# Kernel optimization log

Measured on AMD Instinct MI355X. Metric: run time of the kernel, lower is better.

## Reference

```python
import jax, jax.numpy as jnp
import numpy as np

NUM_ROUTES = 12800   # 32 * 20 * 20
NUM_CAPS = 25
IN_CH = 8
OUT_CH = 64
BATCH = 8
NUM_ITERS = 3


def setup_inputs() -> dict:
    key = jax.random.key(0)
    kx, kw = jax.random.split(key)
    x = jax.random.normal(kx, (BATCH, NUM_ROUTES, IN_CH), dtype=jnp.float32)
    # W parameter: torch shape [1, R, C, O, I] -> store as [R, C, O, I]
    W = jax.random.normal(kw, (NUM_ROUTES, NUM_CAPS, OUT_CH, IN_CH), dtype=jnp.float32)
    return {"x": x, "W": W}


def _squash_elementwise(s):
    # Faithful to source: squared_norm sums over last dim of s_j which has size 1,
    # so squash acts elementwise: s^2 * s / ((1+s^2) * |s|) = s*|s|/(1+s^2).
    sq = s * s
    return sq * s / ((1.0 + sq) * jnp.sqrt(sq))


def reference(x, W):
    # u_hat[b,r,c,o] = sum_i W[r,c,o,i] * x[b,r,i]
    u_hat = jnp.einsum('rcoi,bri->brco', W, x)  # [B, R, C, O]
    b_ij = jnp.zeros((NUM_ROUTES, NUM_CAPS), dtype=x.dtype)
    v = None
    for it in range(NUM_ITERS):
        # legacy F.softmax on 4D [1,R,C,1] uses implicit dim=1 -> over routes
        c_ij = jax.nn.softmax(b_ij, axis=0)                  # [R, C]
        s = jnp.einsum('rc,brco->bco', c_ij, u_hat)          # [B, C, O]
        v = _squash_elementwise(s)
        if it < NUM_ITERS - 1:
            # agreement: <u_hat, v> per (b,r,c), then mean over batch
            a = jnp.einsum('brco,bco->brc', u_hat, v)
            b_ij = b_ij + jnp.mean(a, axis=0)
    # torch returns v_j.squeeze(1) with shape [B, C, O, 1]
    return v[..., None]
```

## Files before the change

kernel.cpp:

```cpp
#include <hip/hip_runtime.h>
#include <cstdint>
#include <cstddef>

#define RN 12800
#define CN 25
#define ON 64
#define IN_ 8
#define BN 8
#define SOUT (BN*CN*ON)

#define RPC 64
#define NRC (RN / RPC)

__device__ __forceinline__ uint32_t pack_bf16(float a, float b) {
    uint32_t ua = __float_as_uint(a);
    uint32_t ub = __float_as_uint(b);
    ua = (ua + 0x7fffu + ((ua >> 16) & 1u)) >> 16;
    ub = (ub + 0x7fffu + ((ub >> 16) & 1u)) & 0xffff0000u;
    return ua | ub;
}
__device__ __forceinline__ float lo_bf16(uint32_t q) { return __uint_as_float(q << 16); }
__device__ __forceinline__ float hi_bf16(uint32_t q) { return __uint_as_float(q & 0xffff0000u); }

__global__ void __launch_bounds__(320, 6)
caps_pass0(const float* __restrict__ x, const float* __restrict__ W,
           float* __restrict__ Sp, uint32_t* __restrict__ U)
{
    __shared__ float xs[RPC][BN][IN_];
    const int chunk = blockIdx.y;
    const int r0 = chunk * RPC;

    for (int t = threadIdx.x; t < RPC * BN * 2; t += 320) {
        const int i4 = t & 1;
        const int rl = (t >> 1) & (RPC - 1);
        const int b  = t >> 7;
        const float4 val = *reinterpret_cast<const float4*>(
            x + (((size_t)b * RN + r0 + rl) * IN_) + i4 * 4);
        *reinterpret_cast<float4*>(&xs[rl][b][i4 * 4]) = val;
    }
    __syncthreads();

    const int wave = threadIdx.x >> 6;
    const int lane = threadIdx.x & 63;
    const int c = blockIdx.x * 5 + wave;

    float acc[BN];
    #pragma unroll
    for (int b = 0; b < BN; ++b) acc[b] = 0.f;

    #pragma unroll 2
    for (int rl = 0; rl < RPC; ++rl) {
        const int r = r0 + rl;
        const float4* wp = reinterpret_cast<const float4*>(
            W + ((((size_t)r * CN + c) * ON + lane) * IN_));
        const float4 w0 = wp[0];
        const float4 w1 = wp[1];

        float u[BN];
        #pragma unroll
        for (int b = 0; b < BN; ++b) {
            const float4 xa = *reinterpret_cast<const float4*>(&xs[rl][b][0]);
            const float4 xb = *reinterpret_cast<const float4*>(&xs[rl][b][4]);
            u[b] = w0.x*xa.x + w0.y*xa.y + w0.z*xa.z + w0.w*xa.w
                 + w1.x*xb.x + w1.y*xb.y + w1.z*xb.z + w1.w*xb.w;
            acc[b] += u[b];
        }

        uint4 q;
        q.x = pack_bf16(u[0], u[1]);
        q.y = pack_bf16(u[2], u[3]);
        q.z = pack_bf16(u[4], u[5]);
        q.w = pack_bf16(u[6], u[7]);
        *reinterpret_cast<uint4*>(U + (((size_t)r * CN + c) * ON + lane) * 4) = q;
    }

    float* sp = Sp + (size_t)chunk * SOUT;
    #pragma unroll
    for (int b = 0; b < BN; ++b)
        sp[(b * CN + c) * ON + lane] = acc[b];
}

template<int MODE>
__global__ void __launch_bounds__(320, 6)
caps_passU(const uint32_t* __restrict__ U, const float* __restrict__ vin,
           const float* __restrict__ bin, float* __restrict__ bout,
           float* __restrict__ Sp, float* __restrict__ Zp)
{
    const int chunk = blockIdx.y;
    const int r0 = chunk * RPC;
    const int wave = threadIdx.x >> 6;
    const int lane = threadIdx.x & 63;
    const int c = blockIdx.x * 5 + wave;

    float vreg[BN];
    #pragma unroll
    for (int b = 0; b < BN; ++b)
        vreg[b] = vin[(b * CN + c) * ON + lane];

    float acc[BN];
    #pragma unroll
    for (int b = 0; b < BN; ++b) acc[b] = 0.f;
    float zacc = 0.f;

    #pragma unroll 2
    for (int rl = 0; rl < RPC; ++rl) {
        const int r = r0 + rl;
        const uint4 q = *reinterpret_cast<const uint4*>(
            U + (((size_t)r * CN + c) * ON + lane) * 4);
        float u[BN];
        u[0] = lo_bf16(q.x); u[1] = hi_bf16(q.x);
        u[2] = lo_bf16(q.y); u[3] = hi_bf16(q.y);
        u[4] = lo_bf16(q.z); u[5] = hi_bf16(q.z);
        u[6] = lo_bf16(q.w); u[7] = hi_bf16(q.w);

        float p = 0.f;
        #pragma unroll
        for (int b = 0; b < BN; ++b) p += u[b] * vreg[b];
        #pragma unroll
        for (int off = 32; off > 0; off >>= 1) p += __shfl_xor(p, off, 64);

        float bn = p * (1.0f / BN);
        if (MODE == 2) bn += bin[(size_t)r * CN + c];
        if (MODE == 1 && lane == 0) bout[(size_t)r * CN + c] = bn;
        const float e = __expf(bn);
        zacc += e;
        #pragma unroll
        for (int b = 0; b < BN; ++b) acc[b] += e * u[b];
    }

    float* sp = Sp + (size_t)chunk * SOUT;
    #pragma unroll
    for (int b = 0; b < BN; ++b)
        sp[(b * CN + c) * ON + lane] = acc[b];
    if (lane == 0)
        Zp[chunk * 32 + c] = zacc;
}

__global__ void caps_zred(const float* __restrict__ Zp, float* __restrict__ z)
{
    __shared__ float l[256];
    const int t = threadIdx.x;
    const int cc = t >> 3;
    const int g  = t & 7;
    float s = 0.f;
    if (cc < CN)
        for (int j = g; j < NRC; j += 8) s += Zp[j * 32 + cc];
    l[t] = s;
    __syncthreads();
    if (g == 0 && cc < CN) {
        float ss = 0.f;
        #pragma unroll
        for (int k = 0; k < 8; ++k) ss += l[cc * 8 + k];
        z[cc] = ss;
    }
}

template<int PASS>
__global__ void __launch_bounds__(256)
caps_fin(const float* __restrict__ Sp, const float* __restrict__ z,
         float* __restrict__ vout)
{
    __shared__ float l[256];
    const int blk = blockIdx.x;
    const int t = threadIdx.x;
    const int o = t & 63;
    const int g = t >> 6;
    const int base = blk * 64 + o;
    float s = 0.f;
    for (int w = g * 50; w < g * 50 + 50; ++w)
        s += Sp[(size_t)w * SOUT + base];
    l[t] = s;
    __syncthreads();
    if (g == 0) {
        float ss = l[o] + l[64 + o] + l[128 + o] + l[192 + o];
        const float zz = (PASS == 0) ? (float)RN : z[blk % CN];
        ss /= zz;
        vout[base] = ss * fabsf(ss) / (1.f + ss * ss);
    }
}

extern "C" void kernel_launch(void* const* d_in, const int* in_sizes, int n_in,
                              void* d_out, int out_size, void* d_ws, size_t ws_size,
                              hipStream_t stream)
{
    const float* x = (const float*)d_in[0];
    const float* W = (const float*)d_in[1];
    float* out = (float*)d_out;
    float* ws = (float*)d_ws;

    float* v  = ws;
    float* z  = v + SOUT;
    float* b1 = z + 32;
    float* Zp = b1 + (size_t)RN * CN;
    float* Sp = Zp + (size_t)NRC * 32;
    uint32_t* U = (uint32_t*)(Sp + (size_t)NRC * SOUT);

    dim3 blk(320), grid(5, NRC);
    dim3 fblk(256), fgrid(BN * CN);

    caps_pass0<<<grid, blk, 0, stream>>>(x, W, Sp, U);
    caps_fin<0><<<fgrid, fblk, 0, stream>>>(Sp, z, v);
    caps_passU<1><<<grid, blk, 0, stream>>>(U, v, nullptr, b1, Sp, Zp);
    caps_zred<<<1, 256, 0, stream>>>(Zp, z);
    caps_fin<1><<<fgrid, fblk, 0, stream>>>(Sp, z, v);
    caps_passU<2><<<grid, blk, 0, stream>>>(U, v, b1, nullptr, Sp, Zp);
    caps_zred<<<1, 256, 0, stream>>>(Zp, z);
    caps_fin<2><<<fgrid, fblk, 0, stream>>>(Sp, z, out);
}
```

Baseline: 384.1 us.

## Fuse all routing passes into one cooperative persistent kernel with grid syncs

Replaces the eight separate kernel launches with a single cooperative persistent kernel that runs the pass0, finalize and routing phases in a grid-stride loop, separated by grid.sync(). The z-normalizer reduction is folded into the finalize phase. W and U accesses now use nontemporal loads and stores. The aim is to remove launch gaps and tail effects between the short phases, at the cost of grid-wide barriers and limited occupancy. A multi-kernel fallback is kept.

```diff
diff --git a/kernel.cpp b/kernel.cpp
--- a/kernel.cpp
+++ b/kernel.cpp
@@ -1,6 +1,9 @@
 #include <hip/hip_runtime.h>
+#include <hip/hip_cooperative_groups.h>
 #include <cstdint>
 #include <cstddef>
+
+namespace cg = cooperative_groups;
 
 #define RN 12800
 #define CN 25
@@ -11,6 +14,11 @@
 
 #define RPC 64
 #define NRC (RN / RPC)
+#define NWU (5 * NRC)
+#define NFIN (BN * CN)
+
+typedef float    f4x  __attribute__((ext_vector_type(4)));
+typedef uint32_t u4x  __attribute__((ext_vector_type(4)));
 
 __device__ __forceinline__ uint32_t pack_bf16(float a, float b) {
     uint32_t ua = __float_as_uint(a);
@@ -22,161 +30,198 @@
 __device__ __forceinline__ float lo_bf16(uint32_t q) { return __uint_as_float(q << 16); }
 __device__ __forceinline__ float hi_bf16(uint32_t q) { return __uint_as_float(q & 0xffff0000u); }
 
-__global__ void __launch_bounds__(320, 6)
-caps_pass0(const float* __restrict__ x, const float* __restrict__ W,
-           float* __restrict__ Sp, uint32_t* __restrict__ U)
-{
-    __shared__ float xs[RPC][BN][IN_];
-    const int chunk = blockIdx.y;
-    const int r0 = chunk * RPC;
-
-    for (int t = threadIdx.x; t < RPC * BN * 2; t += 320) {
-        const int i4 = t & 1;
-        const int rl = (t >> 1) & (RPC - 1);
-        const int b  = t >> 7;
-        const float4 val = *reinterpret_cast<const float4*>(
-            x + (((size_t)b * RN + r0 + rl) * IN_) + i4 * 4);
-        *reinterpret_cast<float4*>(&xs[rl][b][i4 * 4]) = val;
-    }
-    __syncthreads();
-
-    const int wave = threadIdx.x >> 6;
-    const int lane = threadIdx.x & 63;
-    const int c = blockIdx.x * 5 + wave;
-
-    float acc[BN];
-    #pragma unroll
-    for (int b = 0; b < BN; ++b) acc[b] = 0.f;
-
-    #pragma unroll 2
-    for (int rl = 0; rl < RPC; ++rl) {
-        const int r = r0 + rl;
-        const float4* wp = reinterpret_cast<const float4*>(
-            W + ((((size_t)r * CN + c) * ON + lane) * IN_));
-        const float4 w0 = wp[0];
-        const float4 w1 = wp[1];
-
-        float u[BN];
-        #pragma unroll
-        for (int b = 0; b < BN; ++b) {
-            const float4 xa = *reinterpret_cast<const float4*>(&xs[rl][b][0]);
-            const float4 xb = *reinterpret_cast<const float4*>(&xs[rl][b][4]);
-            u[b] = w0.x*xa.x + w0.y*xa.y + w0.z*xa.z + w0.w*xa.w
-                 + w1.x*xb.x + w1.y*xb.y + w1.z*xb.z + w1.w*xb.w;
-            acc[b] += u[b];
-        }
-
-        uint4 q;
-        q.x = pack_bf16(u[0], u[1]);
-        q.y = pack_bf16(u[2], u[3]);
-        q.z = pack_bf16(u[4], u[5]);
-        q.w = pack_bf16(u[6], u[7]);
-        *reinterpret_cast<uint4*>(U + (((size_t)r * CN + c) * ON + lane) * 4) = q;
-    }
-
-    float* sp = Sp + (size_t)chunk * SOUT;
-    #pragma unroll
-    for (int b = 0; b < BN; ++b)
-        sp[(b * CN + c) * ON + lane] = acc[b];
+union SMem {
+    float xs[RPC][BN][IN_];
+    float red[320];
+};
+
+__device__ __forceinline__ void phase_pass0(
+    const float* __restrict__ x, const float* __restrict__ W,
+    float* __restrict__ Sp, uint32_t* __restrict__ U,
+    SMem& sm, int nb, int bid)
+{
+    const int t = threadIdx.x, wave = t >> 6, lane = t & 63;
+    for (int wu = bid; wu < NWU; wu += nb) {
+        const int chunk = wu % NRC, bx = wu / NRC;
+        const int r0 = chunk * RPC;
+        const int c = bx * 5 + wave;
+        __syncthreads();
+        for (int s = t; s < RPC * BN * 2; s += 320) {
+            const int i4 = s & 1, rl = (s >> 1) & (RPC - 1), b = s >> 7;
+            *reinterpret_cast<float4*>(&sm.xs[rl][b][i4 * 4]) =
+                *reinterpret_cast<const float4*>(
+                    x + (((size_t)b * RN + r0 + rl) * IN_) + i4 * 4);
+        }
+        __syncthreads();
+
+        float acc[BN];
+        #pragma unroll
+        for (int b = 0; b < BN; ++b) acc[b] = 0.f;
+
+        #pragma unroll 2
+        for (int rl = 0; rl < RPC; ++rl) {
+            const int r = r0 + rl;
+            const f4x* wp = reinterpret_cast<const f4x*>(
+                W + ((((size_t)r * CN + c) * ON + lane) * IN_));
+            const f4x w0 = __builtin_nontemporal_load(wp);
+            const f4x w1 = __builtin_nontemporal_load(wp + 1);
+
+            float u[BN];
+            #pragma unroll
+            for (int b = 0; b < BN; ++b) {
+                const float4 xa = *reinterpret_cast<const float4*>(&sm.xs[rl][b][0]);
+                const float4 xb = *reinterpret_cast<const float4*>(&sm.xs[rl][b][4]);
+                u[b] = w0.x*xa.x + w0.y*xa.y + w0.z*xa.z + w0.w*xa.w
+                     + w1.x*xb.x + w1.y*xb.y + w1.z*xb.z + w1.w*xb.w;
+                acc[b] += u[b];
+            }
+            u4x q;
+            q.x = pack_bf16(u[0], u[1]);
+            q.y = pack_bf16(u[2], u[3]);
+            q.z = pack_bf16(u[4], u[5]);
+            q.w = pack_bf16(u[6], u[7]);
+            __builtin_nontemporal_store(q, reinterpret_cast<u4x*>(
+                U + (((size_t)r * CN + c) * ON + lane) * 4));
+        }
+        float* sp = Sp + (size_t)chunk * SOUT;
+        #pragma unroll
+        for (int b = 0; b < BN; ++b)
+            sp[(b * CN + c) * ON + lane] = acc[b];
+    }
 }
 
 template<int MODE>
-__global__ void __launch_bounds__(320, 6)
-caps_passU(const uint32_t* __restrict__ U, const float* __restrict__ vin,
-           const float* __restrict__ bin, float* __restrict__ bout,
-           float* __restrict__ Sp, float* __restrict__ Zp)
-{
-    const int chunk = blockIdx.y;
-    const int r0 = chunk * RPC;
-    const int wave = threadIdx.x >> 6;
-    const int lane = threadIdx.x & 63;
-    const int c = blockIdx.x * 5 + wave;
-
-    float vreg[BN];
-    #pragma unroll
-    for (int b = 0; b < BN; ++b)
-        vreg[b] = vin[(b * CN + c) * ON + lane];
-
-    float acc[BN];
-    #pragma unroll
-    for (int b = 0; b < BN; ++b) acc[b] = 0.f;
-    float zacc = 0.f;
-
-    #pragma unroll 2
-    for (int rl = 0; rl < RPC; ++rl) {
-        const int r = r0 + rl;
-        const uint4 q = *reinterpret_cast<const uint4*>(
-            U + (((size_t)r * CN + c) * ON + lane) * 4);
-        float u[BN];
-        u[0] = lo_bf16(q.x); u[1] = hi_bf16(q.x);
-        u[2] = lo_bf16(q.y); u[3] = hi_bf16(q.y);
-        u[4] = lo_bf16(q.z); u[5] = hi_bf16(q.z);
-        u[6] = lo_bf16(q.w); u[7] = hi_bf16(q.w);
-
-        float p = 0.f;
-        #pragma unroll
-        for (int b = 0; b < BN; ++b) p += u[b] * vreg[b];
-        #pragma unroll
-        for (int off = 32; off > 0; off >>= 1) p += __shfl_xor(p, off, 64);
-
-        float bn = p * (1.0f / BN);
-        if (MODE == 2) bn += bin[(size_t)r * CN + c];
-        if (MODE == 1 && lane == 0) bout[(size_t)r * CN + c] = bn;
-        const float e = __expf(bn);
-        zacc += e;
-        #pragma unroll
-        for (int b = 0; b < BN; ++b) acc[b] += e * u[b];
-    }
-
-    float* sp = Sp + (size_t)chunk * SOUT;
-    #pragma unroll
-    for (int b = 0; b < BN; ++b)
-        sp[(b * CN + c) * ON + lane] = acc[b];
-    if (lane == 0)
-        Zp[chunk * 32 + c] = zacc;
-}
-
-__global__ void caps_zred(const float* __restrict__ Zp, float* __restrict__ z)
-{
-    __shared__ float l[256];
-    const int t = threadIdx.x;
-    const int cc = t >> 3;
-    const int g  = t & 7;
-    float s = 0.f;
-    if (cc < CN)
-        for (int j = g; j < NRC; j += 8) s += Zp[j * 32 + cc];
-    l[t] = s;
-    __syncthreads();
-    if (g == 0 && cc < CN) {
-        float ss = 0.f;
-        #pragma unroll
-        for (int k = 0; k < 8; ++k) ss += l[cc * 8 + k];
-        z[cc] = ss;
+__device__ __forceinline__ void phase_passU(
+    const uint32_t* __restrict__ U, const float* __restrict__ vin,
+    const float* __restrict__ bin, float* __restrict__ bout,
+    float* __restrict__ Sp, float* __restrict__ Zp, int nb, int bid)
+{
+    const int t = threadIdx.x, wave = t >> 6, lane = t & 63;
+    for (int wu = bid; wu < NWU; wu += nb) {
+        const int chunk = wu % NRC, bx = wu / NRC;
+        const int r0 = chunk * RPC;
+        const int c = bx * 5 + wave;
+
+        float vreg[BN];
+        #pragma unroll
+        for (int b = 0; b < BN; ++b)
+            vreg[b] = vin[(b * CN + c) * ON + lane];
+
+        float acc[BN];
+        #pragma unroll
+        for (int b = 0; b < BN; ++b) acc[b] = 0.f;
+        float zacc = 0.f;
+
+        #pragma unroll 2
+        for (int rl = 0; rl < RPC; ++rl) {
+            const int r = r0 + rl;
+            const u4x q = __builtin_nontemporal_load(reinterpret_cast<const u4x*>(
+                U + (((size_t)r * CN + c) * ON + lane) * 4));
+            float u[BN];
+            u[0] = lo_bf16(q.x); u[1] = hi_bf16(q.x);
+            u[2] = lo_bf16(q.y); u[3] = hi_bf16(q.y);
+            u[4] = lo_bf16(q.z); u[5] = hi_bf16(q.z);
+            u[6] = lo_bf16(q.w); u[7] = hi_bf16(q.w);
+
+            float p = 0.f;
+            #pragma unroll
+            for (int b = 0; b < BN; ++b) p += u[b] * vreg[b];
+            #pragma unroll
+            for (int off = 32; off > 0; off >>= 1) p += __shfl_xor(p, off, 64);
+
+            float bn = p * (1.0f / BN);
+            if (MODE == 2) bn += bin[(size_t)r * CN + c];
+            if (MODE == 1 && lane == 0) bout[(size_t)r * CN + c] = bn;
+            const float e = __expf(bn);
+            zacc += e;
+            #pragma unroll
+            for (int b = 0; b < BN; ++b) acc[b] += e * u[b];
+        }
+        float* sp = Sp + (size_t)chunk * SOUT;
+        #pragma unroll
+        for (int b = 0; b < BN; ++b)
+            sp[(b * CN + c) * ON + lane] = acc[b];
+        if (lane == 0)
+            Zp[chunk * 32 + c] = zacc;
     }
 }
 
 template<int PASS>
-__global__ void __launch_bounds__(256)
-caps_fin(const float* __restrict__ Sp, const float* __restrict__ z,
-         float* __restrict__ vout)
-{
-    __shared__ float l[256];
-    const int blk = blockIdx.x;
-    const int t = threadIdx.x;
-    const int o = t & 63;
-    const int g = t >> 6;
-    const int base = blk * 64 + o;
-    float s = 0.f;
-    for (int w = g * 50; w < g * 50 + 50; ++w)
-        s += Sp[(size_t)w * SOUT + base];
-    l[t] = s;
-    __syncthreads();
-    if (g == 0) {
-        float ss = l[o] + l[64 + o] + l[128 + o] + l[192 + o];
-        const float zz = (PASS == 0) ? (float)RN : z[blk % CN];
-        ss /= zz;
-        vout[base] = ss * fabsf(ss) / (1.f + ss * ss);
-    }
+__device__ __forceinline__ void phase_fin(
+    const float* __restrict__ Sp, const float* __restrict__ Zp,
+    float* __restrict__ vout, SMem& sm, int nb, int bid)
+{
+    const int t = threadIdx.x, lane = t & 63, g = t >> 6;
+    for (int wu = bid; wu < NFIN; wu += nb) {
+        const int c = wu % CN;
+        float z = (float)RN;
+        if (PASS >= 1) {
+            float zp = 0.f;
+            for (int j = lane; j < NRC; j += 64) zp += Zp[j * 32 + c];
+            #pragma unroll
+            for (int off = 32; off > 0; off >>= 1) zp += __shfl_xor(zp, off, 64);
+            z = zp;
+        }
+        const int base = wu * ON + lane;
+        float s = 0.f;
+        for (int ch = g * 40; ch < g * 40 + 40; ++ch)
+            s += Sp[(size_t)ch * SOUT + base];
+        __syncthreads();
+        sm.red[t] = s;
+        __syncthreads();
+        if (g == 0) {
+            float ss = sm.red[lane] + sm.red[64 + lane] + sm.red[128 + lane]
+                     + sm.red[192 + lane] + sm.red[256 + lane];
+            ss /= z;
+            vout[base] = ss * fabsf(ss) / (1.f + ss * ss);
+        }
+    }
+}
+
+__global__ void __launch_bounds__(320)
+caps_fused(const float* __restrict__ x, const float* __restrict__ W,
+           float* __restrict__ out, float* __restrict__ v, float* __restrict__ b1,
+           float* __restrict__ Zp, float* __restrict__ Sp, uint32_t* __restrict__ U)
+{
+    __shared__ SMem sm;
+    cg::grid_group grid = cg::this_grid();
+    const int nb = gridDim.x, bid = blockIdx.x;
+
+    phase_pass0(x, W, Sp, U, sm, nb, bid);
+    grid.sync();
+    phase_fin<0>(Sp, Zp, v, sm, nb, bid);
+    grid.sync();
+    phase_passU<1>(U, v, nullptr, b1, Sp, Zp, nb, bid);
+    grid.sync();
+    phase_fin<1>(Sp, Zp, v, sm, nb, bid);
+    grid.sync();
+    phase_passU<2>(U, v, b1, nullptr, Sp, Zp, nb, bid);
+    grid.sync();
+    phase_fin<2>(Sp, Zp, out, sm, nb, bid);
+}
+
+__global__ void __launch_bounds__(320)
+k_pass0(const float* __restrict__ x, const float* __restrict__ W,
+        float* __restrict__ Sp, uint32_t* __restrict__ U)
+{
+    __shared__ SMem sm;
+    phase_pass0(x, W, Sp, U, sm, gridDim.x, blockIdx.x);
+}
+template<int MODE>
+__global__ void __launch_bounds__(320)
+k_passU(const uint32_t* __restrict__ U, const float* __restrict__ vin,
+        const float* __restrict__ bin, float* __restrict__ bout,
+        float* __restrict__ Sp, float* __restrict__ Zp)
+{
+    phase_passU<MODE>(U, vin, bin, bout, Sp, Zp, gridDim.x, blockIdx.x);
+}
+template<int PASS>
+__global__ void __launch_bounds__(320)
+k_fin(const float* __restrict__ Sp, const float* __restrict__ Zp,
+      float* __restrict__ vout)
+{
+    __shared__ SMem sm;
+    phase_fin<PASS>(Sp, Zp, vout, sm, gridDim.x, blockIdx.x);
 }
 
 extern "C" void kernel_launch(void* const* d_in, const int* in_sizes, int n_in,
@@ -189,21 +234,32 @@
     float* ws = (float*)d_ws;
 
     float* v  = ws;
-    float* z  = v + SOUT;
-    float* b1 = z + 32;
+    float* b1 = v + SOUT;
     float* Zp = b1 + (size_t)RN * CN;
     float* Sp = Zp + (size_t)NRC * 32;
     uint32_t* U = (uint32_t*)(Sp + (size_t)NRC * SOUT);
 
-    dim3 blk(320), grid(5, NRC);
-    dim3 fblk(256), fgrid(BN * CN);
-
-    caps_pass0<<<grid, blk, 0, stream>>>(x, W, Sp, U);
-    caps_fin<0><<<fgrid, fblk, 0, stream>>>(Sp, z, v);
-    caps_passU<1><<<grid, blk, 0, stream>>>(U, v, nullptr, b1, Sp, Zp);
-    caps_zred<<<1, 256, 0, stream>>>(Zp, z);
-    caps_fin<1><<<fgrid, fblk, 0, stream>>>(Sp, z, v);
-    caps_passU<2><<<grid, blk, 0, stream>>>(U, v, b1, nullptr, Sp, Zp);
-    caps_zred<<<1, 256, 0, stream>>>(Zp, z);
-    caps_fin<2><<<fgrid, fblk, 0, stream>>>(Sp, z, out);
-}
+    int occ = 0;
+    hipError_t err = hipOccupancyMaxActiveBlocksPerMultiprocessor(
+        &occ, reinterpret_cast<const void*>(&caps_fused), 320, 0);
+    bool coop = (err == hipSuccess && occ >= 1);
+    int grid = occ * 256;
+    if (grid > NWU) grid = NWU;
+
+    if (coop) {
+        void* args[8] = { (void*)&x, (void*)&W, (void*)&out, (void*)&v,
+                          (void*)&b1, (void*)&Zp, (void*)&Sp, (void*)&U };
+        err = hipLaunchCooperativeKernel(reinterpret_cast<const void*>(&caps_fused),
+                                         dim3(grid), dim3(320), args, 0, stream);
+        coop = (err == hipSuccess);
+    }
+    if (!coop) {
+        dim3 blk(320), pg(NWU), fg(NFIN);
+        k_pass0<<<pg, blk, 0, stream>>>(x, W, Sp, U);
+        k_fin<0><<<fg, blk, 0, stream>>>(Sp, Zp, v);
+        k_passU<1><<<pg, blk, 0, stream>>>(U, v, nullptr, b1, Sp, Zp);
+        k_fin<1><<<fg, blk, 0, stream>>>(Sp, Zp, v);
+        k_passU<2><<<pg, blk, 0, stream>>>(U, v, b1, nullptr, Sp, Zp);
+        k_fin<2><<<fg, blk, 0, stream>>>(Sp, Zp, out);
+    }
+}
```

After: 682.1 us. 1.78x slower.

## Replace per-chunk partial sums with atomics and fuse squash into routing passes

Applied to the files above, without the earlier changes.

Each routing pass now accumulates its s and z partial sums straight into a single global buffer with float atomics, where before it wrote per-chunk partials that separate reduction kernels summed afterwards. The squash of the previous iteration is folded into the start of the next pass, so the fin and zred kernels go away, leaving one small zero-init kernel and one final squash kernel. This cuts kernel launches and the writes and reads of the 200-chunk partial buffers. In exchange it adds atomic contention on 12800 output addresses and makes the floating-point summation order nondeterministic.

```diff
diff --git a/kernel.cpp b/kernel.cpp
--- a/kernel.cpp
+++ b/kernel.cpp
@@ -22,9 +22,20 @@
 __device__ __forceinline__ float lo_bf16(uint32_t q) { return __uint_as_float(q << 16); }
 __device__ __forceinline__ float hi_bf16(uint32_t q) { return __uint_as_float(q & 0xffff0000u); }
 
+__device__ __forceinline__ float squashf(float s) {
+    return s * fabsf(s) / (1.f + s * s);
+}
+
+#define NZERO (3 * SOUT + 64)
+__global__ void kzero(float* __restrict__ p)
+{
+    const int i = blockIdx.x * blockDim.x + threadIdx.x;
+    if (i < NZERO) p[i] = 0.f;
+}
+
 __global__ void __launch_bounds__(320, 6)
 caps_pass0(const float* __restrict__ x, const float* __restrict__ W,
-           float* __restrict__ Sp, uint32_t* __restrict__ U)
+           float* __restrict__ S0, uint32_t* __restrict__ U)
 {
     __shared__ float xs[RPC][BN][IN_];
     const int chunk = blockIdx.y;
@@ -65,7 +76,6 @@
                  + w1.x*xb.x + w1.y*xb.y + w1.z*xb.z + w1.w*xb.w;
             acc[b] += u[b];
         }
-
         uint4 q;
         q.x = pack_bf16(u[0], u[1]);
         q.y = pack_bf16(u[2], u[3]);
@@ -74,17 +84,17 @@
         *reinterpret_cast<uint4*>(U + (((size_t)r * CN + c) * ON + lane) * 4) = q;
     }
 
-    float* sp = Sp + (size_t)chunk * SOUT;
     #pragma unroll
     for (int b = 0; b < BN; ++b)
-        sp[(b * CN + c) * ON + lane] = acc[b];
+        unsafeAtomicAdd(&S0[(b * CN + c) * ON + lane], acc[b]);
 }
 
 template<int MODE>
 __global__ void __launch_bounds__(320, 6)
-caps_passU(const uint32_t* __restrict__ U, const float* __restrict__ vin,
-           const float* __restrict__ bin, float* __restrict__ bout,
-           float* __restrict__ Sp, float* __restrict__ Zp)
+caps_passU(const uint32_t* __restrict__ U,
+           const float* __restrict__ Sprev, const float* __restrict__ zprev,
+           float* __restrict__ Snext, float* __restrict__ znext,
+           float* __restrict__ b1)
 {
     const int chunk = blockIdx.y;
     const int r0 = chunk * RPC;
@@ -92,10 +102,13 @@
     const int lane = threadIdx.x & 63;
     const int c = blockIdx.x * 5 + wave;
 
+    const float zz = (MODE == 1) ? (float)RN : zprev[c];
     float vreg[BN];
     #pragma unroll
-    for (int b = 0; b < BN; ++b)
-        vreg[b] = vin[(b * CN + c) * ON + lane];
+    for (int b = 0; b < BN; ++b) {
+        const float sv = Sprev[(b * CN + c) * ON + lane] / zz;
+        vreg[b] = squashf(sv);
+    }
 
     float acc[BN];
     #pragma unroll
@@ -120,63 +133,29 @@
         for (int off = 32; off > 0; off >>= 1) p += __shfl_xor(p, off, 64);
 
         float bn = p * (1.0f / BN);
-        if (MODE == 2) bn += bin[(size_t)r * CN + c];
-        if (MODE == 1 && lane == 0) bout[(size_t)r * CN + c] = bn;
+        if (MODE == 2) bn += b1[(size_t)r * CN + c];
+        if (MODE == 1 && lane == 0) b1[(size_t)r * CN + c] = bn;
         const float e = __expf(bn);
         zacc += e;
         #pragma unroll
         for (int b = 0; b < BN; ++b) acc[b] += e * u[b];
     }
 
-    float* sp = Sp + (size_t)chunk * SOUT;
     #pragma unroll
     for (int b = 0; b < BN; ++b)
-        sp[(b * CN + c) * ON + lane] = acc[b];
+        unsafeAtomicAdd(&Snext[(b * CN + c) * ON + lane], acc[b]);
     if (lane == 0)
-        Zp[chunk * 32 + c] = zacc;
+        unsafeAtomicAdd(&znext[c], zacc);
 }
 
-__global__ void caps_zred(const float* __restrict__ Zp, float* __restrict__ z)
+__global__ void caps_sqfin(const float* __restrict__ S2, const float* __restrict__ zb,
+                           float* __restrict__ out)
 {
-    __shared__ float l[256];
-    const int t = threadIdx.x;
-    const int cc = t >> 3;
-    const int g  = t & 7;
-    float s = 0.f;
-    if (cc < CN)
-        for (int j = g; j < NRC; j += 8) s += Zp[j * 32 + cc];
-    l[t] = s;
-    __syncthreads();
-    if (g == 0 && cc < CN) {
-        float ss = 0.f;
-        #pragma unroll
-        for (int k = 0; k < 8; ++k) ss += l[cc * 8 + k];
-        z[cc] = ss;
-    }
-}
-
-template<int PASS>
-__global__ void __launch_bounds__(256)
-caps_fin(const float* __restrict__ Sp, const float* __restrict__ z,
-         float* __restrict__ vout)
-{
-    __shared__ float l[256];
-    const int blk = blockIdx.x;
-    const int t = threadIdx.x;
-    const int o = t & 63;
-    const int g = t >> 6;
-    const int base = blk * 64 + o;
-    float s = 0.f;
-    for (int w = g * 50; w < g * 50 + 50; ++w)
-        s += Sp[(size_t)w * SOUT + base];
-    l[t] = s;
-    __syncthreads();
-    if (g == 0) {
-        float ss = l[o] + l[64 + o] + l[128 + o] + l[192 + o];
-        const float zz = (PASS == 0) ? (float)RN : z[blk % CN];
-        ss /= zz;
-        vout[base] = ss * fabsf(ss) / (1.f + ss * ss);
-    }
+    const int idx = blockIdx.x * blockDim.x + threadIdx.x;
+    if (idx >= SOUT) return;
+    const int c = (idx >> 6) % CN;
+    const float s = S2[idx] / zb[c];
+    out[idx] = squashf(s);
 }
 
 extern "C" void kernel_launch(void* const* d_in, const int* in_sizes, int n_in,
@@ -188,22 +167,19 @@
     float* out = (float*)d_out;
     float* ws = (float*)d_ws;
 
-    float* v  = ws;
-    float* z  = v + SOUT;
-    float* b1 = z + 32;
-    float* Zp = b1 + (size_t)RN * CN;
-    float* Sp = Zp + (size_t)NRC * 32;
-    uint32_t* U = (uint32_t*)(Sp + (size_t)NRC * SOUT);
+    float* S0 = ws;
+    float* S1 = S0 + SOUT;
+    float* S2 = S1 + SOUT;
+    float* za = S2 + SOUT;
+    float* zb = za + 32;
+    float* b1 = zb + 32;
+    uint32_t* U = (uint32_t*)(b1 + (size_t)RN * CN);
 
     dim3 blk(320), grid(5, NRC);
-    dim3 fblk(256), fgrid(BN * CN);
 
-    caps_pass0<<<grid, blk, 0, stream>>>(x, W, Sp, U);
-    caps_fin<0><<<fgrid, fblk, 0, stream>>>(Sp, z, v);
-    caps_passU<1><<<grid, blk, 0, stream>>>(U, v, nullptr, b1, Sp, Zp);
-    caps_zred<<<1, 256, 0, stream>>>(Zp, z);
-    caps_fin<1><<<fgrid, fblk, 0, stream>>>(Sp, z, v);
-    caps_passU<2><<<grid, blk, 0, stream>>>(U, v, b1, nullptr, Sp, Zp);
-    caps_zred<<<1, 256, 0, stream>>>(Zp, z);
-    caps_fin<2><<<fgrid, fblk, 0, stream>>>(Sp, z, out);
+    kzero<<<(NZERO + 255) / 256, 256, 0, stream>>>(S0);
+    caps_pass0<<<grid, blk, 0, stream>>>(x, W, S0, U);
+    caps_passU<1><<<grid, blk, 0, stream>>>(U, S0, nullptr, S1, za, b1);
+    caps_passU<2><<<grid, blk, 0, stream>>>(U, S1, za, S2, zb, b1);
+    caps_sqfin<<<(SOUT + 255) / 256, 256, 0, stream>>>(S2, zb, out);
 }
```

Measured after the change: 423.2 us. 1.1x slower.
